# Optimization experiments

Measured on AMD Instinct MI355X. Metric: run time of the kernel, lower is better.

## Reference

```python
import jax, jax.numpy as jnp
import numpy as np

T, K = 3, 3  # filter_size = [T, K, K]
PAD = K // 2


def setup_inputs() -> dict:
    key = jax.random.key(0)
    k1, k2 = jax.random.split(key)
    B, H, W, C_out = 8, 192, 192, 16
    x = jax.random.normal(k1, (B, T, H, W), dtype=jnp.float32)
    f = jax.random.normal(k2, (B, H, W, T * K * K, C_out), dtype=jnp.float32)
    return {"x": x, "f": f}


def _im2col(x):
    # x: (B, T, H, W) -> patches (B, H, W, K*K*T), channel order (kh, kw, t)
    # matching eye(27).reshape(K, K, T, 27) used as a TF HWIO conv filter
    # with SAME padding.
    B, Tt, H, W = x.shape
    xp = jnp.pad(x, ((0, 0), (0, 0), (PAD, PAD), (PAD, PAD)))
    cols = [xp[:, t, i:i + H, j:j + W]
            for i in range(K) for j in range(K) for t in range(Tt)]
    return jnp.stack(cols, axis=-1)  # (B, H, W, K*K*T)


def reference(x, f):
    # per-pixel dynamic filtering: out[b,h,w,o] = sum_k patches[b,h,w,k] * f[b,h,w,k,o]
    patches = _im2col(x)  # (B, H, W, 27)
    return jnp.einsum('bhwk,bhwko->bhwo', patches, f)  # (B, H, W, C_out)
```

## Files before the change

### kernel.cpp

```cpp
#include <hip/hip_runtime.h>


#define B_ 8
#define T_ 3
#define H_ 192
#define W_ 192
#define CO_ 16
#define KT_ 27
#define PIX_PER_BLK 32
#define HALO_W 34
#define XS_N (3 * 3 * HALO_W)
#define PL_N (PIX_PER_BLK * KT_)

__global__ __launch_bounds__(256) void DynFilter3D_kernel(
    const float* __restrict__ x,
    const float* __restrict__ f,
    float* __restrict__ out)
{
    int blk = blockIdx.x;
    int wt  = blk % 6;
    int bh  = blk / 6;
    int h   = bh % H_;
    int b   = bh / H_;
    int w0  = wt * PIX_PER_BLK;

    __shared__ float xs[XS_N];
    __shared__ float pl[PL_N];

    for (int idx = threadIdx.x; idx < XS_N; idx += 256) {
        int wp = idx % HALO_W;
        int ti = idx / HALO_W;
        int i  = ti % 3;
        int t  = ti / 3;
        int hh = h + i - 1;
        int ww = w0 + wp - 1;
        float v = 0.0f;
        if ((unsigned)hh < (unsigned)H_ && (unsigned)ww < (unsigned)W_)
            v = x[(size_t)((b * T_ + t) * H_ + hh) * W_ + ww];
        xs[idx] = v;
    }
    __syncthreads();

    for (int idx = threadIdx.x; idx < PL_N; idx += 256) {
        int k  = idx % KT_;
        int pxl = idx / KT_;
        int t  = k % 3;
        int ij = k / 3;
        int jw = ij % 3;
        int i  = ij / 3;
        pl[idx] = xs[(t * 3 + i) * HALO_W + pxl + jw];
    }
    __syncthreads();

    int wl = threadIdx.x >> 3;
    int j  = threadIdx.x & 7;
    int k0 = j >> 2;
    size_t pix = (size_t)(b * H_ + h) * W_ + w0 + wl;

    const float4* fb = reinterpret_cast<const float4*>(f + pix * (KT_ * CO_));
    const float*  pp = pl + wl * KT_ + k0;

    float4 acc = make_float4(0.f, 0.f, 0.f, 0.f);
#pragma unroll
    for (int m = 0; m < 14; ++m) {
        int e = j + 8 * m;
        if (e < KT_ * 4) {
            float4 fv = fb[e];
            float  p  = pp[2 * m];
            acc.x = fmaf(p, fv.x, acc.x);
            acc.y = fmaf(p, fv.y, acc.y);
            acc.z = fmaf(p, fv.z, acc.z);
            acc.w = fmaf(p, fv.w, acc.w);
        }
    }

    acc.x += __shfl_xor(acc.x, 4);
    acc.y += __shfl_xor(acc.y, 4);
    acc.z += __shfl_xor(acc.z, 4);
    acc.w += __shfl_xor(acc.w, 4);

    if (j < 4)
        reinterpret_cast<float4*>(out + pix * CO_)[j] = acc;
}

extern "C" void kernel_launch(void* const* d_in, const int* in_sizes, int n_in,
                              void* d_out, int out_size, void* d_ws, size_t ws_size,
                              hipStream_t stream) {
    const float* x = (const float*)d_in[0];
    const float* f = (const float*)d_in[1];
    float* out = (float*)d_out;

    const int grid = B_ * H_ * (W_ / PIX_PER_BLK);
    DynFilter3D_kernel<<<grid, 256, 0, stream>>>(x, f, out);
}
```

Before: 97.19 us.

## Process full image row per block and read taps directly from shared halo

```diff
diff --git a/kernel.cpp b/kernel.cpp
--- a/kernel.cpp
+++ b/kernel.cpp
@@ -7,10 +7,13 @@
 #define W_ 192
 #define CO_ 16
 #define KT_ 27
-#define PIX_PER_BLK 32
-#define HALO_W 34
-#define XS_N (3 * 3 * HALO_W)
-#define PL_N (PIX_PER_BLK * KT_)
+#define HALO_W 194
+#define XS_N (9 * HALO_W)
+
+__host__ __device__ constexpr int tap_off(int k) {
+    int t = k % 3, ij = k / 3, i = ij / 3, jw = ij % 3;
+    return (t * 3 + i) * HALO_W + jw;
+}
 
 __global__ __launch_bounds__(256) void DynFilter3D_kernel(
     const float* __restrict__ x,
@@ -18,14 +21,10 @@
     float* __restrict__ out)
 {
     int blk = blockIdx.x;
-    int wt  = blk % 6;
-    int bh  = blk / 6;
-    int h   = bh % H_;
-    int b   = bh / H_;
-    int w0  = wt * PIX_PER_BLK;
+    int h   = blk % H_;
+    int b   = blk / H_;
 
     __shared__ float xs[XS_N];
-    __shared__ float pl[PL_N];
 
     for (int idx = threadIdx.x; idx < XS_N; idx += 256) {
         int wp = idx % HALO_W;
@@ -33,7 +32,7 @@
         int i  = ti % 3;
         int t  = ti / 3;
         int hh = h + i - 1;
-        int ww = w0 + wp - 1;
+        int ww = wp - 1;
         float v = 0.0f;
         if ((unsigned)hh < (unsigned)H_ && (unsigned)ww < (unsigned)W_)
             v = x[(size_t)((b * T_ + t) * H_ + hh) * W_ + ww];
@@ -41,46 +40,45 @@
     }
     __syncthreads();
 
-    for (int idx = threadIdx.x; idx < PL_N; idx += 256) {
-        int k  = idx % KT_;
-        int pxl = idx / KT_;
-        int t  = k % 3;
-        int ij = k / 3;
-        int jw = ij % 3;
-        int i  = ij / 3;
-        pl[idx] = xs[(t * 3 + i) * HALO_W + pxl + jw];
-    }
-    __syncthreads();
-
     int wl = threadIdx.x >> 3;
     int j  = threadIdx.x & 7;
     int k0 = j >> 2;
-    size_t pix = (size_t)(b * H_ + h) * W_ + w0 + wl;
+    size_t rowbase = (size_t)(b * H_ + h) * W_;
 
-    const float4* fb = reinterpret_cast<const float4*>(f + pix * (KT_ * CO_));
-    const float*  pp = pl + wl * KT_ + k0;
+#pragma unroll 1
+    for (int seg = 0; seg < W_ / 32; ++seg) {
+        int w = seg * 32 + wl;
+        size_t pix = rowbase + w;
+        const float4* fb = reinterpret_cast<const float4*>(f + pix * (KT_ * CO_));
+        const float*  xb = xs + w;
 
-    float4 acc = make_float4(0.f, 0.f, 0.f, 0.f);
+        float4 acc = make_float4(0.f, 0.f, 0.f, 0.f);
 #pragma unroll
-    for (int m = 0; m < 14; ++m) {
-        int e = j + 8 * m;
-        if (e < KT_ * 4) {
-            float4 fv = fb[e];
-            float  p  = pp[2 * m];
-            acc.x = fmaf(p, fv.x, acc.x);
-            acc.y = fmaf(p, fv.y, acc.y);
-            acc.z = fmaf(p, fv.z, acc.z);
-            acc.w = fmaf(p, fv.w, acc.w);
+        for (int m = 0; m < 14; ++m) {
+            int e = j + 8 * m;
+            if (e < KT_ * 4) {
+                float4 fv = fb[e];
+                constexpr int KE = 1;
+                (void)KE;
+                int offE = tap_off(2 * m);
+                int offO = tap_off((2 * m + 1 < KT_) ? 2 * m + 1 : 2 * m);
+                int off  = k0 ? offO : offE;
+                float p  = xb[off];
+                acc.x = fmaf(p, fv.x, acc.x);
+                acc.y = fmaf(p, fv.y, acc.y);
+                acc.z = fmaf(p, fv.z, acc.z);
+                acc.w = fmaf(p, fv.w, acc.w);
+            }
         }
+
+        acc.x += __shfl_xor(acc.x, 4);
+        acc.y += __shfl_xor(acc.y, 4);
+        acc.z += __shfl_xor(acc.z, 4);
+        acc.w += __shfl_xor(acc.w, 4);
+
+        if (j < 4)
+            reinterpret_cast<float4*>(out + pix * CO_)[j] = acc;
     }
-
-    acc.x += __shfl_xor(acc.x, 4);
-    acc.y += __shfl_xor(acc.y, 4);
-    acc.z += __shfl_xor(acc.z, 4);
-    acc.w += __shfl_xor(acc.w, 4);
-
-    if (j < 4)
-        reinterpret_cast<float4*>(out + pix * CO_)[j] = acc;
 }
 
 extern "C" void kernel_launch(void* const* d_in, const int* in_sizes, int n_in,
@@ -90,6 +88,6 @@
     const float* f = (const float*)d_in[1];
     float* out = (float*)d_out;
 
-    const int grid = B_ * H_ * (W_ / PIX_PER_BLK);
+    const int grid = B_ * H_;
     DynFilter3D_kernel<<<grid, 256, 0, stream>>>(x, f, out);
 }
```

Measured after the change: 109.3 us. +12.5%, slower.
